# Optimization experiments

Hardware: AMD Instinct MI355X
Metric: run time of the kernel (lower is better)

## Reference

```python
import jax, jax.numpy as jnp
import numpy as np

DIM = 1024
HEADS = 16
HEAD_DIM = DIM // HEADS

def setup_inputs() -> dict:
    key = jax.random.key(0)
    ks = jax.random.split(key, 6)
    s = 0.02
    return {
        "x": jax.random.normal(ks[0], (2, 2048, DIM), dtype=jnp.float32),
        "w_qkv": jax.random.normal(ks[1], (DIM, 3 * DIM), dtype=jnp.float32) * s,
        "w_proj": jax.random.normal(ks[2], (DIM, DIM), dtype=jnp.float32) * s,
        "b_proj": jnp.zeros((DIM,), dtype=jnp.float32),
        "ln_gamma": jnp.ones((DIM,), dtype=jnp.float32),
        "ln_beta": jnp.zeros((DIM,), dtype=jnp.float32),
    }

def layer_norm(x, gamma, beta, eps=1e-5):
    mu = jnp.mean(x, axis=-1, keepdims=True)
    var = jnp.var(x, axis=-1, keepdims=True)
    return (x - mu) * jax.lax.rsqrt(var + eps) * gamma + beta

def reference(x, w_qkv, w_proj, b_proj, ln_gamma, ln_beta):
    B, N, C = x.shape
    residual = x
    h = layer_norm(x, ln_gamma, ln_beta)
    qkv = h @ w_qkv  # [B,N,3C]
    qkv = qkv.reshape(B, N, 3, HEADS, HEAD_DIM)
    q = jnp.transpose(qkv[:, :, 0], (0, 2, 1, 3))  # [B,H,N,D]
    k = jnp.transpose(qkv[:, :, 1], (0, 2, 1, 3))
    v = jnp.transpose(qkv[:, :, 2], (0, 2, 1, 3))
    scale = 1.0 / jnp.sqrt(jnp.float32(HEAD_DIM))
    attn = jnp.einsum('bhqd,bhkd->bhqk', q, k) * scale
    attn = jax.nn.softmax(attn, axis=-1)
    out = jnp.einsum('bhqk,bhkd->bhqd', attn, v)  # [B,H,N,D]
    out = jnp.transpose(out, (0, 2, 1, 3)).reshape(B, N, C)
    out = out @ w_proj + b_proj
    return out + residual
```

## Files before the change

### kernel.cpp

```cpp
#include <hip/hip_runtime.h>

#define DIM   1024
#define HEADS 16
#define HDIM  64
#define BATCH 2
#define SEQ   2048
#define TOK   (BATCH*SEQ)
#define MEG   1048576

typedef __bf16 bf16x8 __attribute__((ext_vector_type(8)));
typedef float  f32x4  __attribute__((ext_vector_type(4)));
typedef float  f32x16 __attribute__((ext_vector_type(16)));

__device__ __forceinline__ float b2f(ushort u) {
    union { unsigned int u32; float f; } x; x.u32 = ((unsigned int)u) << 16; return x.f;
}
__device__ __forceinline__ ushort f2b(float f) {
    union { float f; unsigned int u32; } x; x.f = f;
    unsigned int r = x.u32 + 0x7FFFu + ((x.u32 >> 16) & 1u);
    return (ushort)(r >> 16);
}
__device__ __forceinline__ void gload_lds16(const ushort* g, void* l) {
    __builtin_amdgcn_global_load_lds((const __attribute__((address_space(1))) void*)g,
                                     (__attribute__((address_space(3))) void*)l, 16, 0, 0);
}
__device__ __forceinline__ float fexp2(float x) {
    float r; asm("v_exp_f32 %0, %1" : "=v"(r) : "v"(x)); return r;
}
__device__ __forceinline__ unsigned int cvtpk_bf16(float lo, float hi) {
    unsigned int r; asm("v_cvt_pk_bf16_f32 %0, %1, %2" : "=v"(r) : "v"(lo), "v"(hi)); return r;
}
__device__ __forceinline__ void plane32swap(unsigned int &a, unsigned int &b) {
    asm("v_permlane32_swap_b32 %0, %1" : "+v"(a), "+v"(b));
}
__device__ __forceinline__ bf16x8 pack8(float e0, float e1, float e2, float e3,
                                        float e4, float e5, float e6, float e7) {
    unsigned int a = cvtpk_bf16(e0, e1), b = cvtpk_bf16(e2, e3);
    unsigned int c = cvtpk_bf16(e4, e5), d = cvtpk_bf16(e6, e7);
    plane32swap(a, c); plane32swap(b, d);
    union { unsigned int u[4]; bf16x8 v; } r;
    r.u[0] = a; r.u[1] = b; r.u[2] = c; r.u[3] = d;
    return r.v;
}

__global__ void transpose_f2b_k(const float* __restrict__ src, ushort* __restrict__ dst,
                                int R, int Cc) {
    __shared__ ushort tile[32][33];
    int c0 = blockIdx.x * 32, r0 = blockIdx.y * 32;
    int tx = threadIdx.x, ty = threadIdx.y;
#pragma unroll
    for (int i = 0; i < 4; i++)
        tile[ty + 8 * i][tx] = f2b(src[(long)(r0 + ty + 8 * i) * Cc + c0 + tx]);
    __syncthreads();
#pragma unroll
    for (int i = 0; i < 4; i++)
        dst[(long)(c0 + ty + 8 * i) * R + r0 + tx] = tile[tx][ty + 8 * i];
}

__global__ __launch_bounds__(256)
void ln_k(const float* __restrict__ x, const float* __restrict__ gamma,
          const float* __restrict__ beta, ushort* __restrict__ h) {
    __shared__ float red[8];
    int row = blockIdx.x, tid = threadIdx.x;
    const float* xr = x + (long)row * DIM;
    float4 xv = *(const float4*)(xr + tid * 4);
    float s1 = xv.x + xv.y + xv.z + xv.w;
    float s2 = xv.x * xv.x + xv.y * xv.y + xv.z * xv.z + xv.w * xv.w;
#pragma unroll
    for (int off = 32; off; off >>= 1) {
        s1 += __shfl_down(s1, off);
        s2 += __shfl_down(s2, off);
    }
    int wid = tid >> 6, lane = tid & 63;
    if (lane == 0) { red[wid * 2] = s1; red[wid * 2 + 1] = s2; }
    __syncthreads();
    s1 = red[0] + red[2] + red[4] + red[6];
    s2 = red[1] + red[3] + red[5] + red[7];
    float mu  = s1 * (1.0f / DIM);
    float var = s2 * (1.0f / DIM) - mu * mu;
    float rs  = rsqrtf(var + 1e-5f);
    float4 gv = *(const float4*)(gamma + tid * 4);
    float4 bv = *(const float4*)(beta + tid * 4);
    ushort4 ov;
    ov.x = f2b((xv.x - mu) * rs * gv.x + bv.x);
    ov.y = f2b((xv.y - mu) * rs * gv.y + bv.y);
    ov.z = f2b((xv.z - mu) * rs * gv.z + bv.z);
    ov.w = f2b((xv.w - mu) * rs * gv.w + bv.w);
    *(ushort4*)(h + (long)row * DIM + tid * 4) = ov;
}

__global__ __launch_bounds__(256, 3)
void gemm_qkv_k(const ushort* __restrict__ A, const ushort* __restrict__ Bt,
                ushort* __restrict__ qp, ushort* __restrict__ kp, ushort* __restrict__ vp) {
    __shared__ ushort smem[16384];
    int tid  = threadIdx.x;
    int wid  = tid >> 6, lane = tid & 63;
    int quad = lane >> 4, l16 = lane & 15;
    int wm = wid >> 1, wn = wid & 1;
    int rowbase = blockIdx.y * 128;
    int colbase = blockIdx.x * 128;

    f32x4 acc[4][4];
#pragma unroll
    for (int i = 0; i < 4; i++)
#pragma unroll
        for (int j = 0; j < 4; j++) acc[i][j] = (f32x4){0.f, 0.f, 0.f, 0.f};

    for (int k0 = 0; k0 < DIM; k0 += 64) {
#pragma unroll
        for (int p = 0; p < 2; p++) {
            int c = wid * 2 + p;
            int r = c * 16 + (lane >> 2);
            int ac = (lane & 3) * 8;
#pragma unroll
            for (int pnl = 0; pnl < 2; pnl++) {
                int cc = k0 + pnl * 32 + ac;
                gload_lds16(A  + (long)(rowbase + r) * DIM + cc,
                            &smem[pnl * 4096 + c * 16 * 32]);
                gload_lds16(Bt + (long)(colbase + r) * DIM + cc,
                            &smem[8192 + pnl * 4096 + c * 16 * 32]);
            }
        }
        __syncthreads();
#pragma unroll
        for (int pnl = 0; pnl < 2; pnl++) {
            bf16x8 fa[4], fb[4];
#pragma unroll
            for (int t = 0; t < 4; t++)
                fa[t] = *(const bf16x8*)(&smem[pnl * 4096 + (wm * 64 + t * 16 + l16) * 32 + quad * 8]);
#pragma unroll
            for (int t = 0; t < 4; t++)
                fb[t] = *(const bf16x8*)(&smem[8192 + pnl * 4096 + (wn * 64 + t * 16 + l16) * 32 + quad * 8]);
#pragma unroll
            for (int i = 0; i < 4; i++)
#pragma unroll
                for (int j = 0; j < 4; j++)
                    acc[i][j] = __builtin_amdgcn_mfma_f32_16x16x32_bf16(fa[i], fb[j], acc[i][j], 0, 0, 0);
        }
        __syncthreads();
    }

    if (colbase >= 2048) {
#pragma unroll
        for (int i = 0; i < 4; i++)
#pragma unroll
            for (int j = 0; j < 4; j++) {
                int cl = wn * 64 + j * 16 + l16;
                int rl = wm * 64 + i * 16 + quad * 4;
#pragma unroll
                for (int r = 0; r < 4; r++)
                    smem[cl * 128 + rl + r] = f2b(acc[i][j][r]);
            }
        __syncthreads();
        int b = rowbase >> 11, nnb = rowbase & 2047;
        int hbase = (colbase - 2048) >> 6;
#pragma unroll
        for (int i = 0; i < 8; i++) {
            int id = i * 256 + tid;
            int cl = id >> 4;
            int off = (id & 15) * 8;
            int hh = hbase + (cl >> 6), d = cl & 63;
            uint4 val = *(const uint4*)(&smem[cl * 128 + off]);
            *(uint4*)(vp + (((long)b * HEADS + hh) * HDIM + d) * SEQ + nnb + off) = val;
        }
    } else {
#pragma unroll
        for (int i = 0; i < 4; i++)
#pragma unroll
            for (int j = 0; j < 4; j++) {
                int m0  = rowbase + wm * 64 + i * 16 + quad * 4;
                int col = colbase + wn * 64 + j * 16 + l16;
                int part = col >> 10, rem = col & 1023;
                int head = rem >> 6, d = rem & 63;
                ushort* dst = (part == 0) ? qp : kp;
#pragma unroll
                for (int r = 0; r < 4; r++) {
                    float v = acc[i][j][r];
                    int mm = m0 + r;
                    int b = mm >> 11, nn = mm & 2047;
                    float sv = (part == 0) ? v * 0.18033688011f : v;
                    dst[((((long)b * HEADS + head) * SEQ + nn) << 6) + d] = f2b(sv);
                }
            }
    }
}

__global__ __launch_bounds__(256, 3)
void gemm_proj_k(const ushort* __restrict__ A, const ushort* __restrict__ Bt,
                 const float* __restrict__ bias, const float* __restrict__ xres,
                 float* __restrict__ outp) {
    __shared__ ushort As[2][128][32];
    __shared__ ushort Bs[2][64][32];
    int tid  = threadIdx.x;
    int wid  = tid >> 6, lane = tid & 63;
    int quad = lane >> 4, l16 = lane & 15;
    int rowbase = blockIdx.y * 128;
    int colbase = blockIdx.x * 64;
    int arow = lane >> 2, acol = (lane & 3) * 8;

    f32x4 acc[2][4];
#pragma unroll
    for (int i = 0; i < 2; i++)
#pragma unroll
        for (int j = 0; j < 4; j++) acc[i][j] = (f32x4){0.f, 0.f, 0.f, 0.f};

    for (int k0 = 0; k0 < DIM; k0 += 64) {
#pragma unroll
        for (int p = 0; p < 2; p++) {
            int c = wid * 2 + p;
            int r = c * 16 + arow;
            int mm = rowbase + r;
            int bq = mm >> 11, nn = mm & 2047;
#pragma unroll
            for (int pnl = 0; pnl < 2; pnl++) {
                int cc = k0 + pnl * 32 + acol;
                int head = cc >> 6, d = cc & 63;
                gload_lds16(A + ((((long)bq * HEADS + head) * SEQ + nn) << 6) + d,
                            &As[pnl][c * 16][0]);
            }
        }
        {
            int r = wid * 16 + arow;
#pragma unroll
            for (int pnl = 0; pnl < 2; pnl++) {
                int cc = k0 + pnl * 32 + acol;
                gload_lds16(Bt + (long)(colbase + r) * DIM + cc, &Bs[pnl][wid * 16][0]);
            }
        }
        __syncthreads();
#pragma unroll
        for (int pnl = 0; pnl < 2; pnl++) {
            bf16x8 fa[2], fb[4];
#pragma unroll
            for (int t = 0; t < 2; t++)
                fa[t] = *(const bf16x8*)(&As[pnl][wid * 32 + t * 16 + l16][quad * 8]);
#pragma unroll
            for (int t = 0; t < 4; t++)
                fb[t] = *(const bf16x8*)(&Bs[pnl][t * 16 + l16][quad * 8]);
#pragma unroll
            for (int i = 0; i < 2; i++)
#pragma unroll
                for (int j = 0; j < 4; j++)
                    acc[i][j] = __builtin_amdgcn_mfma_f32_16x16x32_bf16(fa[i], fb[j], acc[i][j], 0, 0, 0);
        }
        __syncthreads();
    }

#pragma unroll
    for (int i = 0; i < 2; i++)
#pragma unroll
        for (int j = 0; j < 4; j++) {
            int m0  = rowbase + wid * 32 + i * 16 + quad * 4;
            int col = colbase + j * 16 + l16;
#pragma unroll
            for (int r = 0; r < 4; r++) {
                int mm = m0 + r;
                outp[(long)mm * DIM + col] = acc[i][j][r] + bias[col] + xres[(long)mm * DIM + col];
            }
        }
}

__global__ __launch_bounds__(256, 2)
void attn_k(ushort* qio, const ushort* __restrict__ kg,
            const ushort* __restrict__ vt) {
    __shared__ __align__(16) ushort Kp[2][4096];
    __shared__ __align__(16) ushort Vs[2][4096];
    int bh = blockIdx.y;
    int tid = threadIdx.x, wid = tid >> 6;
    int lane = tid & 63;
    int l31 = lane & 31, hi = lane >> 5;
    ushort* qh = qio + (long)bh * SEQ * HDIM;
    const ushort* kh = kg + (long)bh * SEQ * HDIM;
    const ushort* vh = vt + (long)bh * HDIM * SEQ;

    int srow = tid >> 3, schk = tid & 7;
    int sofs = srow * 64 + ((schk ^ (srow & 7)) * 8);
    const ushort* kbase = kh + (long)srow * HDIM + schk * 8;
    const ushort* vbase = vh + (long)srow * SEQ + schk * 8;

    int qrow0 = blockIdx.x * 128 + wid * 32;
    bf16x8 qf[4];
#pragma unroll
    for (int ks = 0; ks < 4; ks++)
        qf[ks] = *(const bf16x8*)(qh + (long)(qrow0 + l31) * HDIM + ks * 16 + hi * 8);

    f32x16 o0 = {}, o1 = {};
    f32x4 lac = {0.f, 0.f, 0.f, 0.f};

    uint4 kr0 = *(const uint4*)(kbase);
    uint4 kr1 = *(const uint4*)(kbase + 32 * HDIM);
    uint4 vr0 = *(const uint4*)(vbase);
    uint4 vr1 = *(const uint4*)(vbase + 32 * SEQ);
    *(uint4*)(&Kp[0][sofs])        = kr0;
    *(uint4*)(&Kp[0][sofs + 2048]) = kr1;
    *(uint4*)(&Vs[0][sofs])        = vr0;
    *(uint4*)(&Vs[0][sofs + 2048]) = vr1;

    const int NIT = SEQ / 64;
    for (int it = 0; it < NIT; ++it) {
        int buf = it & 1;
        __syncthreads();
        if (it + 1 < NIT) {
            int kt = (it + 1) * 64;
            kr0 = *(const uint4*)(kbase + (long)kt * HDIM);
            kr1 = *(const uint4*)(kbase + (long)(kt + 32) * HDIM);
            vr0 = *(const uint4*)(vbase + kt);
            vr1 = *(const uint4*)(vbase + 32 * SEQ + kt);
        }

        f32x16 sc0 = {}, sc1 = {};
        __builtin_amdgcn_s_setprio(1);
#pragma unroll
        for (int ks = 0; ks < 4; ks++) {
            int psl = ((2 * ks + hi) ^ (l31 & 7)) * 8;
            bf16x8 ka = *(const bf16x8*)(&Kp[buf][l31 * 64 + psl]);
            bf16x8 kb = *(const bf16x8*)(&Kp[buf][(32 + l31) * 64 + psl]);
            sc0 = __builtin_amdgcn_mfma_f32_32x32x16_bf16(ka, qf[ks], sc0, 0, 0, 0);
            sc1 = __builtin_amdgcn_mfma_f32_32x32x16_bf16(kb, qf[ks], sc1, 0, 0, 0);
        }
        __builtin_amdgcn_s_setprio(0);

        float e0[16], e1[16];
#pragma unroll
        for (int r = 0; r < 16; r++) { e0[r] = fexp2(sc0[r]); e1[r] = fexp2(sc1[r]); }
#pragma unroll
        for (int r = 0; r < 4; r++)
            lac += (f32x4){e0[4*r], e0[4*r+1], e0[4*r+2], e0[4*r+3]}
                 + (f32x4){e1[4*r], e1[4*r+1], e1[4*r+2], e1[4*r+3]};

        bf16x8 pa0 = pack8(e0[0], e0[1], e0[2],  e0[3],  e0[4],  e0[5],  e0[6],  e0[7]);
        bf16x8 pa1 = pack8(e0[8], e0[9], e0[10], e0[11], e0[12], e0[13], e0[14], e0[15]);
        bf16x8 pa2 = pack8(e1[0], e1[1], e1[2],  e1[3],  e1[4],  e1[5],  e1[6],  e1[7]);
        bf16x8 pa3 = pack8(e1[8], e1[9], e1[10], e1[11], e1[12], e1[13], e1[14], e1[15]);

        __builtin_amdgcn_s_setprio(1);
#pragma unroll
        for (int g = 0; g < 4; g++) {
            int psl = ((2 * g + hi) ^ (l31 & 7)) * 8;
            bf16x8 v0 = *(const bf16x8*)(&Vs[buf][l31 * 64 + psl]);
            bf16x8 v1 = *(const bf16x8*)(&Vs[buf][(32 + l31) * 64 + psl]);
            bf16x8 pg = (g == 0) ? pa0 : (g == 1) ? pa1 : (g == 2) ? pa2 : pa3;
            o0 = __builtin_amdgcn_mfma_f32_32x32x16_bf16(pg, v0, o0, 0, 0, 0);
            o1 = __builtin_amdgcn_mfma_f32_32x32x16_bf16(pg, v1, o1, 0, 0, 0);
        }
        __builtin_amdgcn_s_setprio(0);

        if (it + 1 < NIT) {
            *(uint4*)(&Kp[buf ^ 1][sofs])        = kr0;
            *(uint4*)(&Kp[buf ^ 1][sofs + 2048]) = kr1;
            *(uint4*)(&Vs[buf ^ 1][sofs])        = vr0;
            *(uint4*)(&Vs[buf ^ 1][sofs + 2048]) = vr1;
        }
    }

    float t = lac[0] + lac[1] + lac[2] + lac[3];
    t += __shfl_xor(t, 32);
    float linv = 1.0f / t;
#pragma unroll
    for (int r = 0; r < 16; r++) {
        int qrow = (r & 3) + 8 * (r >> 2) + 4 * hi;
        float lr = __shfl(linv, qrow);
        long ro = (long)(qrow0 + qrow) * HDIM;
        qh[ro + l31]      = f2b(o0[r] * lr);
        qh[ro + 32 + l31] = f2b(o1[r] * lr);
    }
}

extern "C" void kernel_launch(void* const* d_in, const int* in_sizes, int n_in,
                              void* d_out, int out_size, void* d_ws, size_t ws_size,
                              hipStream_t stream) {
    const float* x      = (const float*)d_in[0];
    const float* w_qkv  = (const float*)d_in[1];
    const float* w_proj = (const float*)d_in[2];
    const float* b_proj = (const float*)d_in[3];
    const float* gamma  = (const float*)d_in[4];
    const float* beta   = (const float*)d_in[5];
    float* out = (float*)d_out;

    ushort* ws   = (ushort*)d_ws;
    ushort* h    = ws;
    ushort* wqt  = ws + (size_t)4 * MEG;
    ushort* qb   = ws + (size_t)7 * MEG;
    ushort* kb   = ws + (size_t)11 * MEG;
    ushort* vtb  = ws + (size_t)15 * MEG;

    transpose_f2b_k<<<dim3(3 * DIM / 32, DIM / 32), dim3(32, 8), 0, stream>>>(
        w_qkv, wqt, DIM, 3 * DIM);
    ln_k<<<dim3(TOK), dim3(256), 0, stream>>>(x, gamma, beta, h);
    gemm_qkv_k<<<dim3(3 * DIM / 128, TOK / 128), dim3(256), 0, stream>>>(
        h, wqt, qb, kb, vtb);
    attn_k<<<dim3(SEQ / 128, BATCH * HEADS), dim3(256), 0, stream>>>(qb, kb, vtb);
    transpose_f2b_k<<<dim3(DIM / 32, DIM / 32), dim3(32, 8), 0, stream>>>(
        w_proj, kb, DIM, DIM);
    gemm_proj_k<<<dim3(DIM / 64, TOK / 128), dim3(256), 0, stream>>>(
        qb, kb, b_proj, x, out);
}
```

Baseline: 190.3 us.

## Software-pipeline attention: overlap next QK^T with current softmax and PV

Switches the attention loop from a double-buffered to a triple-buffered LDS ring of K/V tiles. It software-pipelines the loop so the QK^T MFMAs for tile t+1 are issued before the exp/pack and PV MFMAs for tile t, letting matrix and transcendental work overlap. Global prefetch now runs two tiles ahead. The cost is 48KB of LDS per block instead of 32KB and more live accumulator registers, which may reduce occupancy under the 2-blocks-per-CU launch bound.

Result: no change. 188.5 us (-1.0%).

```diff
diff --git a/kernel.cpp b/kernel.cpp
--- a/kernel.cpp
+++ b/kernel.cpp
@@ -41,6 +41,15 @@
     union { unsigned int u[4]; bf16x8 v; } r;
     r.u[0] = a; r.u[1] = b; r.u[2] = c; r.u[3] = d;
     return r.v;
+}
+__device__ __forceinline__ bf16x8 exp_pack8(const f32x16 &sc, int base, f32x4 &lac) {
+    float e0 = fexp2(sc[base + 0]), e1 = fexp2(sc[base + 1]);
+    float e2 = fexp2(sc[base + 2]), e3 = fexp2(sc[base + 3]);
+    float e4 = fexp2(sc[base + 4]), e5 = fexp2(sc[base + 5]);
+    float e6 = fexp2(sc[base + 6]), e7 = fexp2(sc[base + 7]);
+    lac += (f32x4){e0, e1, e2, e3};
+    lac += (f32x4){e4, e5, e6, e7};
+    return pack8(e0, e1, e2, e3, e4, e5, e6, e7);
 }
 
 __global__ void transpose_f2b_k(const float* __restrict__ src, ushort* __restrict__ dst,
@@ -263,8 +272,7 @@
 __global__ __launch_bounds__(256, 2)
 void attn_k(ushort* qio, const ushort* __restrict__ kg,
             const ushort* __restrict__ vt) {
-    __shared__ __align__(16) ushort Kp[2][4096];
-    __shared__ __align__(16) ushort Vs[2][4096];
+    __shared__ __align__(16) ushort lds[3 * 8192];
     int bh = blockIdx.y;
     int tid = threadIdx.x, wid = tid >> 6;
     int lane = tid & 63;
@@ -287,70 +295,97 @@
     f32x16 o0 = {}, o1 = {};
     f32x4 lac = {0.f, 0.f, 0.f, 0.f};
 
-    uint4 kr0 = *(const uint4*)(kbase);
-    uint4 kr1 = *(const uint4*)(kbase + 32 * HDIM);
-    uint4 vr0 = *(const uint4*)(vbase);
-    uint4 vr1 = *(const uint4*)(vbase + 32 * SEQ);
-    *(uint4*)(&Kp[0][sofs])        = kr0;
-    *(uint4*)(&Kp[0][sofs + 2048]) = kr1;
-    *(uint4*)(&Vs[0][sofs])        = vr0;
-    *(uint4*)(&Vs[0][sofs + 2048]) = vr1;
+    {
+        uint4 a0 = *(const uint4*)(kbase);
+        uint4 a1 = *(const uint4*)(kbase + 32 * HDIM);
+        uint4 b0 = *(const uint4*)(vbase);
+        uint4 b1 = *(const uint4*)(vbase + 32 * SEQ);
+        uint4 c0 = *(const uint4*)(kbase + 64 * HDIM);
+        uint4 c1 = *(const uint4*)(kbase + 96 * HDIM);
+        uint4 d0 = *(const uint4*)(vbase + 64);
+        uint4 d1 = *(const uint4*)(vbase + 32 * SEQ + 64);
+        *(uint4*)(&lds[sofs])               = a0;
+        *(uint4*)(&lds[sofs + 2048])        = a1;
+        *(uint4*)(&lds[4096 + sofs])        = b0;
+        *(uint4*)(&lds[4096 + sofs + 2048]) = b1;
+        *(uint4*)(&lds[8192 + sofs])               = c0;
+        *(uint4*)(&lds[8192 + sofs + 2048])        = c1;
+        *(uint4*)(&lds[8192 + 4096 + sofs])        = d0;
+        *(uint4*)(&lds[8192 + 4096 + sofs + 2048]) = d1;
+    }
+    __syncthreads();
+
+    f32x16 sc0 = {}, sc1 = {};
+    __builtin_amdgcn_s_setprio(1);
+#pragma unroll
+    for (int ks = 0; ks < 4; ks++) {
+        int psl = ((2 * ks + hi) ^ (l31 & 7)) * 8;
+        bf16x8 ka = *(const bf16x8*)(&lds[l31 * 64 + psl]);
+        bf16x8 kb = *(const bf16x8*)(&lds[(32 + l31) * 64 + psl]);
+        sc0 = __builtin_amdgcn_mfma_f32_32x32x16_bf16(ka, qf[ks], sc0, 0, 0, 0);
+        sc1 = __builtin_amdgcn_mfma_f32_32x32x16_bf16(kb, qf[ks], sc1, 0, 0, 0);
+    }
+    __builtin_amdgcn_s_setprio(0);
 
     const int NIT = SEQ / 64;
-    for (int it = 0; it < NIT; ++it) {
-        int buf = it & 1;
-        __syncthreads();
-        if (it + 1 < NIT) {
-            int kt = (it + 1) * 64;
+    int s0 = 0, s1 = 1, s2 = 2;
+    for (int t = 0; t < NIT; ++t) {
+        uint4 kr0, kr1, vr0, vr1;
+        bool stage = (t + 2 < NIT);
+        if (stage) {
+            int kt = (t + 2) * 64;
             kr0 = *(const uint4*)(kbase + (long)kt * HDIM);
             kr1 = *(const uint4*)(kbase + (long)(kt + 32) * HDIM);
             vr0 = *(const uint4*)(vbase + kt);
             vr1 = *(const uint4*)(vbase + 32 * SEQ + kt);
         }
 
-        f32x16 sc0 = {}, sc1 = {};
-        __builtin_amdgcn_s_setprio(1);
-#pragma unroll
-        for (int ks = 0; ks < 4; ks++) {
-            int psl = ((2 * ks + hi) ^ (l31 & 7)) * 8;
-            bf16x8 ka = *(const bf16x8*)(&Kp[buf][l31 * 64 + psl]);
-            bf16x8 kb = *(const bf16x8*)(&Kp[buf][(32 + l31) * 64 + psl]);
-            sc0 = __builtin_amdgcn_mfma_f32_32x32x16_bf16(ka, qf[ks], sc0, 0, 0, 0);
-            sc1 = __builtin_amdgcn_mfma_f32_32x32x16_bf16(kb, qf[ks], sc1, 0, 0, 0);
-        }
-        __builtin_amdgcn_s_setprio(0);
-
-        float e0[16], e1[16];
-#pragma unroll
-        for (int r = 0; r < 16; r++) { e0[r] = fexp2(sc0[r]); e1[r] = fexp2(sc1[r]); }
-#pragma unroll
-        for (int r = 0; r < 4; r++)
-            lac += (f32x4){e0[4*r], e0[4*r+1], e0[4*r+2], e0[4*r+3]}
-                 + (f32x4){e1[4*r], e1[4*r+1], e1[4*r+2], e1[4*r+3]};
-
-        bf16x8 pa0 = pack8(e0[0], e0[1], e0[2],  e0[3],  e0[4],  e0[5],  e0[6],  e0[7]);
-        bf16x8 pa1 = pack8(e0[8], e0[9], e0[10], e0[11], e0[12], e0[13], e0[14], e0[15]);
-        bf16x8 pa2 = pack8(e1[0], e1[1], e1[2],  e1[3],  e1[4],  e1[5],  e1[6],  e1[7]);
-        bf16x8 pa3 = pack8(e1[8], e1[9], e1[10], e1[11], e1[12], e1[13], e1[14], e1[15]);
-
-        __builtin_amdgcn_s_setprio(1);
-#pragma unroll
-        for (int g = 0; g < 4; g++) {
-            int psl = ((2 * g + hi) ^ (l31 & 7)) * 8;
-            bf16x8 v0 = *(const bf16x8*)(&Vs[buf][l31 * 64 + psl]);
-            bf16x8 v1 = *(const bf16x8*)(&Vs[buf][(32 + l31) * 64 + psl]);
-            bf16x8 pg = (g == 0) ? pa0 : (g == 1) ? pa1 : (g == 2) ? pa2 : pa3;
-            o0 = __builtin_amdgcn_mfma_f32_32x32x16_bf16(pg, v0, o0, 0, 0, 0);
-            o1 = __builtin_amdgcn_mfma_f32_32x32x16_bf16(pg, v1, o1, 0, 0, 0);
-        }
-        __builtin_amdgcn_s_setprio(0);
-
-        if (it + 1 < NIT) {
-            *(uint4*)(&Kp[buf ^ 1][sofs])        = kr0;
-            *(uint4*)(&Kp[buf ^ 1][sofs + 2048]) = kr1;
-            *(uint4*)(&Vs[buf ^ 1][sofs])        = vr0;
-            *(uint4*)(&Vs[buf ^ 1][sofs + 2048]) = vr1;
-        }
+        f32x16 n0 = {}, n1 = {};
+        if (t + 1 < NIT) {
+            const ushort* Kb = &lds[s1 * 8192];
+            __builtin_amdgcn_s_setprio(1);
+#pragma unroll
+            for (int ks = 0; ks < 4; ks++) {
+                int psl = ((2 * ks + hi) ^ (l31 & 7)) * 8;
+                bf16x8 ka = *(const bf16x8*)(&Kb[l31 * 64 + psl]);
+                bf16x8 kb = *(const bf16x8*)(&Kb[(32 + l31) * 64 + psl]);
+                n0 = __builtin_amdgcn_mfma_f32_32x32x16_bf16(ka, qf[ks], n0, 0, 0, 0);
+                n1 = __builtin_amdgcn_mfma_f32_32x32x16_bf16(kb, qf[ks], n1, 0, 0, 0);
+            }
+            __builtin_amdgcn_s_setprio(0);
+        }
+
+        bf16x8 pa0 = exp_pack8(sc0, 0, lac);
+        bf16x8 pa1 = exp_pack8(sc0, 8, lac);
+        bf16x8 pa2 = exp_pack8(sc1, 0, lac);
+        bf16x8 pa3 = exp_pack8(sc1, 8, lac);
+
+        {
+            const ushort* Vb = &lds[s0 * 8192 + 4096];
+            __builtin_amdgcn_s_setprio(1);
+#pragma unroll
+            for (int g = 0; g < 4; g++) {
+                int psl = ((2 * g + hi) ^ (l31 & 7)) * 8;
+                bf16x8 v0 = *(const bf16x8*)(&Vb[l31 * 64 + psl]);
+                bf16x8 v1 = *(const bf16x8*)(&Vb[(32 + l31) * 64 + psl]);
+                bf16x8 pg = (g == 0) ? pa0 : (g == 1) ? pa1 : (g == 2) ? pa2 : pa3;
+                o0 = __builtin_amdgcn_mfma_f32_32x32x16_bf16(pg, v0, o0, 0, 0, 0);
+                o1 = __builtin_amdgcn_mfma_f32_32x32x16_bf16(pg, v1, o1, 0, 0, 0);
+            }
+            __builtin_amdgcn_s_setprio(0);
+        }
+
+        if (stage) {
+            ushort* Sb = &lds[s2 * 8192];
+            *(uint4*)(&Sb[sofs])               = kr0;
+            *(uint4*)(&Sb[sofs + 2048])        = kr1;
+            *(uint4*)(&Sb[4096 + sofs])        = vr0;
+            *(uint4*)(&Sb[4096 + sofs + 2048]) = vr1;
+        }
+
+        sc0 = n0; sc1 = n1;
+        int tmp = s0; s0 = s1; s1 = s2; s2 = tmp;
+        __syncthreads();
     }
 
     float t = lac[0] + lac[1] + lac[2] + lac[3];
```

## Stage QKV epilogue through padded LDS and remap attention blocks across XCDs

Applied to the files above, without the earlier changes.

The Q/K epilogue of the QKV GEMM now writes scaled bf16 results into a padded shared-memory tile and then stores them as 16-byte vectors, replacing scattered 2-byte global stores. The V-transpose tile gets padding (stride 136) to reduce LDS bank conflicts. The attention kernel uses a flattened 1D grid with a swizzle so that blocks of the same batch-head land on the same XCD, aiming for better L2 reuse of K/V. The barrier in the attention loop is moved after the next tile's global loads are issued, so those loads overlap the wait. The costs are an extra barrier and LDS round-trip in the GEMM epilogue, plus more LDS per block.

New measurement: 183.5 us. 1.04x faster.

```diff
diff --git a/kernel.cpp b/kernel.cpp
--- a/kernel.cpp
+++ b/kernel.cpp
@@ -92,7 +92,7 @@
 __global__ __launch_bounds__(256, 3)
 void gemm_qkv_k(const ushort* __restrict__ A, const ushort* __restrict__ Bt,
                 ushort* __restrict__ qp, ushort* __restrict__ kp, ushort* __restrict__ vp) {
-    __shared__ ushort smem[16384];
+    __shared__ __align__(16) ushort smem[17408];
     int tid  = threadIdx.x;
     int wid  = tid >> 6, lane = tid & 63;
     int quad = lane >> 4, l16 = lane & 15;
@@ -149,7 +149,7 @@
                 int rl = wm * 64 + i * 16 + quad * 4;
 #pragma unroll
                 for (int r = 0; r < 4; r++)
-                    smem[cl * 128 + rl + r] = f2b(acc[i][j][r]);
+                    smem[cl * 136 + rl + r] = f2b(acc[i][j][r]);
             }
         __syncthreads();
         int b = rowbase >> 11, nnb = rowbase & 2047;
@@ -160,28 +160,36 @@
             int cl = id >> 4;
             int off = (id & 15) * 8;
             int hh = hbase + (cl >> 6), d = cl & 63;
-            uint4 val = *(const uint4*)(&smem[cl * 128 + off]);
+            uint4 val = *(const uint4*)(&smem[cl * 136 + off]);
             *(uint4*)(vp + (((long)b * HEADS + hh) * HDIM + d) * SEQ + nnb + off) = val;
         }
     } else {
+        float s = (colbase < 1024) ? 0.18033688011f : 1.0f;
 #pragma unroll
         for (int i = 0; i < 4; i++)
 #pragma unroll
             for (int j = 0; j < 4; j++) {
-                int m0  = rowbase + wm * 64 + i * 16 + quad * 4;
-                int col = colbase + wn * 64 + j * 16 + l16;
-                int part = col >> 10, rem = col & 1023;
-                int head = rem >> 6, d = rem & 63;
-                ushort* dst = (part == 0) ? qp : kp;
-#pragma unroll
-                for (int r = 0; r < 4; r++) {
-                    float v = acc[i][j][r];
-                    int mm = m0 + r;
-                    int b = mm >> 11, nn = mm & 2047;
-                    float sv = (part == 0) ? v * 0.18033688011f : v;
-                    dst[((((long)b * HEADS + head) * SEQ + nn) << 6) + d] = f2b(sv);
-                }
-            }
+                int rl = wm * 64 + i * 16 + quad * 4;
+                int cl = wn * 64 + j * 16 + l16;
+#pragma unroll
+                for (int r = 0; r < 4; r++)
+                    smem[(rl + r) * 136 + cl] = f2b(acc[i][j][r] * s);
+            }
+        __syncthreads();
+        ushort* dst = (colbase < 1024) ? qp : kp;
+        int cb = colbase & 1023;
+#pragma unroll
+        for (int i = 0; i < 8; i++) {
+            int id = i * 256 + tid;
+            int rl = id >> 4;
+            int ch = id & 15;
+            int col = cb + ch * 8;
+            int head = col >> 6, d = col & 63;
+            int mm = rowbase + rl;
+            int b = mm >> 11, nn = mm & 2047;
+            uint4 val = *(const uint4*)(&smem[rl * 136 + ch * 8]);
+            *(uint4*)(dst + ((((long)b * HEADS + head) * SEQ + nn) << 6) + d) = val;
+        }
     }
 }
 
@@ -265,7 +273,9 @@
             const ushort* __restrict__ vt) {
     __shared__ __align__(16) ushort Kp[2][4096];
     __shared__ __align__(16) ushort Vs[2][4096];
-    int bh = blockIdx.y;
+    int flat = blockIdx.x;
+    int swz  = (flat & 7) * 64 + (flat >> 3);
+    int qx = swz & 15, bh = swz >> 4;
     int tid = threadIdx.x, wid = tid >> 6;
     int lane = tid & 63;
     int l31 = lane & 31, hi = lane >> 5;
@@ -278,7 +288,7 @@
     const ushort* kbase = kh + (long)srow * HDIM + schk * 8;
     const ushort* vbase = vh + (long)srow * SEQ + schk * 8;
 
-    int qrow0 = blockIdx.x * 128 + wid * 32;
+    int qrow0 = qx * 128 + wid * 32;
     bf16x8 qf[4];
 #pragma unroll
     for (int ks = 0; ks < 4; ks++)
@@ -299,7 +309,6 @@
     const int NIT = SEQ / 64;
     for (int it = 0; it < NIT; ++it) {
         int buf = it & 1;
-        __syncthreads();
         if (it + 1 < NIT) {
             int kt = (it + 1) * 64;
             kr0 = *(const uint4*)(kbase + (long)kt * HDIM);
@@ -307,6 +316,7 @@
             vr0 = *(const uint4*)(vbase + kt);
             vr1 = *(const uint4*)(vbase + 32 * SEQ + kt);
         }
+        __syncthreads();
 
         f32x16 sc0 = {}, sc1 = {};
         __builtin_amdgcn_s_setprio(1);
@@ -389,7 +399,7 @@
     ln_k<<<dim3(TOK), dim3(256), 0, stream>>>(x, gamma, beta, h);
     gemm_qkv_k<<<dim3(3 * DIM / 128, TOK / 128), dim3(256), 0, stream>>>(
         h, wqt, qb, kb, vtb);
-    attn_k<<<dim3(SEQ / 128, BATCH * HEADS), dim3(256), 0, stream>>>(qb, kb, vtb);
+    attn_k<<<dim3((SEQ / 128) * BATCH * HEADS), dim3(256), 0, stream>>>(qb, kb, vtb);
     transpose_f2b_k<<<dim3(DIM / 32, DIM / 32), dim3(32, 8), 0, stream>>>(
         w_proj, kb, DIM, DIM);
     gemm_proj_k<<<dim3(DIM / 64, TOK / 128), dim3(256), 0, stream>>>(
```
